# Kernel tuning notes

Hardware: AMD Instinct MI355X
Metric: run time of the kernel (lower is better)

The kernel has to match this reference:

```python
import jax, jax.numpy as jnp
import numpy as np

# ---- static configuration (matches init_kwargs) ----
B = 256              # graph pairs -> 2B graphs total (query/corpus interleaved)
N_PER_GRAPH = 24     # nodes per graph
N_MAX = 32           # max node set size (transport plan side)
E_PER_GRAPH = 200    # edges per graph
E_MAX = 256          # max_edge_set_size
D_EDGE = 256         # edge_feature_dim
D_SINK = 256         # sinkhorn_feature_dim
TEMPERATURE = 0.1
NUM_SINKHORN_ITERS = 20
NOISE_FACTOR = 0.0   # deterministic sinkhorn
CONSISTENCY_WEIGHT = 1.0


def setup_inputs() -> dict:
    rng = np.random.RandomState(0)
    num_graphs = 2 * B
    node_offset = np.arange(num_graphs) * N_PER_GRAPH
    graph_idx = np.repeat(np.arange(num_graphs), N_PER_GRAPH)
    # edges are grouped by graph (standard batched-graph layout)
    from_local = rng.randint(0, N_PER_GRAPH, size=(num_graphs, E_PER_GRAPH))
    to_local = rng.randint(0, N_PER_GRAPH, size=(num_graphs, E_PER_GRAPH))
    from_idx = (from_local + node_offset[:, None]).reshape(-1)
    to_idx = (to_local + node_offset[:, None]).reshape(-1)
    total_edges = num_graphs * E_PER_GRAPH

    key = jax.random.key(0)
    k = jax.random.split(key, 4)
    return {
        "edge_features_enc": jax.random.normal(k[0], (total_edges, D_EDGE), jnp.float32),
        "node_transport_plan": jax.random.uniform(k[1], (B, N_MAX, N_MAX), jnp.float32),
        "W1": jax.random.normal(k[2], (D_EDGE, D_SINK), jnp.float32) / np.sqrt(D_EDGE).astype(np.float32),
        "b1": jnp.zeros((D_SINK,), jnp.float32),
        "W2": jax.random.normal(k[3], (D_SINK, D_SINK), jnp.float32) / np.sqrt(D_SINK).astype(np.float32),
        "b2": jnp.zeros((D_SINK,), jnp.float32),
        "from_idx": jnp.asarray(from_idx, jnp.int32),
        "to_idx": jnp.asarray(to_idx, jnp.int32),
        "graph_idx": jnp.asarray(graph_idx, jnp.int32),
        "query_sizes": jnp.full((B,), N_PER_GRAPH, jnp.int32),
        "corpus_sizes": jnp.full((B,), N_PER_GRAPH, jnp.int32),
    }


def reference(edge_features_enc, node_transport_plan, W1, b1, W2, b2,
              from_idx, to_idx, graph_idx, query_sizes, corpus_sizes):
    num_graphs = 2 * B
    total_edges = from_idx.shape[0]

    # --- get_paired_edge_counts / split_and_stack ---
    g_edge = graph_idx[from_idx]                                   # graph id per edge
    edge_counts = jax.ops.segment_sum(jnp.ones_like(g_edge), g_edge, num_segments=num_graphs)
    edge_offset = jnp.cumsum(edge_counts) - edge_counts            # exclusive prefix
    rank = jnp.arange(total_edges, dtype=jnp.int32) - edge_offset[g_edge]

    stacked = jnp.zeros((num_graphs, E_MAX, D_EDGE), edge_features_enc.dtype)
    stacked = stacked.at[g_edge, rank].set(edge_features_enc)      # [2B, E_MAX, D]
    q_feat, c_feat = stacked[0::2], stacked[1::2]

    # --- sinkhorn_feature_layers (Linear-ReLU-Linear) + size mask ---
    def mlp(x):
        return jax.nn.relu(x @ W1 + b1) @ W2 + b2
    q_feat, c_feat = mlp(q_feat), mlp(c_feat)
    pos = jnp.arange(E_MAX)
    q_feat = q_feat * (pos[None, :] < query_sizes[:, None]).astype(q_feat.dtype)[..., None]
    c_feat = c_feat * (pos[None, :] < corpus_sizes[:, None]).astype(c_feat.dtype)[..., None]

    # --- kronecker_product_on_nodes: local endpoint ids, pad slots -> zero row N_MAX ---
    node_counts = jax.ops.segment_sum(jnp.ones_like(graph_idx), graph_idx, num_segments=num_graphs)
    node_offset = jnp.cumsum(node_counts) - node_counts
    pad = jnp.full((num_graphs, E_MAX), N_MAX, jnp.int32)
    f_loc = pad.at[g_edge, rank].set(from_idx - node_offset[g_edge])
    t_loc = pad.at[g_edge, rank].set(to_idx - node_offset[g_edge])
    fq, fc = f_loc[0::2], f_loc[1::2]
    tq, tc = t_loc[0::2], t_loc[1::2]

    T = jnp.pad(node_transport_plan, ((0, 0), (0, 1), (0, 1)))     # zero row/col for pads
    b = jnp.arange(B)[:, None, None]
    straight = T[b, fq[:, :, None], fc[:, None, :]] * T[b, tq[:, :, None], tc[:, None, :]]
    cross = T[b, fq[:, :, None], tc[:, None, :]] * T[b, tq[:, :, None], fc[:, None, :]]

    # --- sinkhorn_iters (log domain, noise_factor=0) ---
    log_alpha = (straight + cross) / TEMPERATURE                   # [B, E_MAX, E_MAX]
    def step(la, _):
        la = la - jax.nn.logsumexp(la, axis=2, keepdims=True)
        la = la - jax.nn.logsumexp(la, axis=1, keepdims=True)
        return la, None
    log_alpha, _ = jax.lax.scan(step, log_alpha, None, length=NUM_SINKHORN_ITERS)
    plan = jnp.exp(log_alpha)

    # --- feature_alignment_score: -sum(relu(q - P c)) per pair ---
    score = -jax.nn.relu(q_feat - plan @ c_feat).sum(axis=(1, 2))
    return CONSISTENCY_WEIGHT * score
```

## Files before the change

### kernel.cpp

```cpp
#include <hip/hip_runtime.h>

typedef unsigned short ushort_t;
typedef unsigned int uint_t;

typedef float f32x4_t __attribute__((ext_vector_type(4)));
typedef short s16x8_t __attribute__((ext_vector_type(8)));

#define NB   256
#define NG   512
#define NPG  24
#define NMAXI 32
#define EPG  200
#define DD   256
#define L2E_OVER_T 14.426950408889634f

#define PADIDX(i) ((((i) >> 6) * 68) + ((i) & 63))

__device__ __forceinline__ ushort_t f2bf(float f) {
    uint_t u = __float_as_uint(f);
    u += 0x7FFFu + ((u >> 16) & 1u);
    return (ushort_t)(u >> 16);
}
__device__ __forceinline__ float bfhi(uint_t u) { return __uint_as_float(u & 0xFFFF0000u); }
__device__ __forceinline__ float bflo(uint_t u) { return __uint_as_float(u << 16); }

__device__ __forceinline__ float frcp(float x) {
#if __has_builtin(__builtin_amdgcn_rcpf)
    return __builtin_amdgcn_rcpf(x);
#else
    return 1.0f / x;
#endif
}

__global__ __launch_bounds__(256) void prep_w(const float* __restrict__ W1,
                                              const float* __restrict__ W2,
                                              ushort_t* __restrict__ W1T,
                                              ushort_t* __restrict__ W2T)
{
    __shared__ float tile[2][4 * 256];
    const int t = threadIdx.x;
    const int k0 = blockIdx.x * 4;
    #pragma unroll
    for (int i = t; i < 4 * 256; i += 256) {
        tile[0][i] = W1[k0 * 256 + i];
        tile[1][i] = W2[k0 * 256 + i];
    }
    __syncthreads();
    const int n = t;
    #pragma unroll
    for (int m = 0; m < 2; ++m) {
        uint_t p0 = (uint_t)f2bf(tile[m][0 * 256 + n]) | ((uint_t)f2bf(tile[m][1 * 256 + n]) << 16);
        uint_t p1 = (uint_t)f2bf(tile[m][2 * 256 + n]) | ((uint_t)f2bf(tile[m][3 * 256 + n]) << 16);
        ushort_t* dst = (m ? W2T : W1T) + n * 256 + k0;
        uint2 pk; pk.x = p0; pk.y = p1;
        *(uint2*)dst = pk;
    }
}

__global__ __launch_bounds__(256) void mlp_kernel(
    const float* __restrict__ X, const ushort_t* __restrict__ W1T,
    const ushort_t* __restrict__ W2T, const float* __restrict__ b1,
    const float* __restrict__ b2, float* __restrict__ Y)
{
    __shared__ ushort_t sA[64 * 272];
    const int t = threadIdx.x;
    const int blk = blockIdx.x;
    const int lane = t & 63;
    const int w = t >> 6;
    const int quad = lane >> 4;
    const int mrow = lane & 15;

    {
        int r = t >> 2;
        int ch = (t & 3) * 64;
        int rho = blk * 64 + r;
        int g = rho / NPG;
        int e = rho - g * NPG;
        const float* src = X + ((size_t)(g * EPG + e)) * DD + ch;
        ushort_t* dst = &sA[r * 272 + ch];
        #pragma unroll
        for (int i = 0; i < 8; ++i) {
            float4 v0 = *(const float4*)(src + i * 8);
            float4 v1 = *(const float4*)(src + i * 8 + 4);
            uint4 pk;
            pk.x = (uint_t)f2bf(v0.x) | ((uint_t)f2bf(v0.y) << 16);
            pk.y = (uint_t)f2bf(v0.z) | ((uint_t)f2bf(v0.w) << 16);
            pk.z = (uint_t)f2bf(v1.x) | ((uint_t)f2bf(v1.y) << 16);
            pk.w = (uint_t)f2bf(v1.z) | ((uint_t)f2bf(v1.w) << 16);
            *(uint4*)(dst + i * 8) = pk;
        }
    }
    __syncthreads();

    f32x4_t acc[16];
    #pragma unroll
    for (int i = 0; i < 16; ++i) acc[i] = (f32x4_t){0.f, 0.f, 0.f, 0.f};

    #pragma unroll
    for (int k0 = 0; k0 < 256; k0 += 32) {
        s16x8_t a[4], bb[4];
        #pragma unroll
        for (int mt = 0; mt < 4; ++mt)
            a[mt] = *(const s16x8_t*)&sA[(mt * 16 + mrow) * 272 + k0 + quad * 8];
        #pragma unroll
        for (int nt = 0; nt < 4; ++nt)
            bb[nt] = *(const s16x8_t*)(W1T + (size_t)(64 * w + nt * 16 + mrow) * 256 + k0 + quad * 8);
        #pragma unroll
        for (int mt = 0; mt < 4; ++mt) {
            #pragma unroll
            for (int nt = 0; nt < 4; ++nt)
                acc[mt * 4 + nt] = __builtin_amdgcn_mfma_f32_16x16x32_bf16(
                    a[mt], bb[nt], acc[mt * 4 + nt], 0, 0, 0);
        }
    }
    __syncthreads();

    #pragma unroll
    for (int nt = 0; nt < 4; ++nt) {
        int col = 64 * w + nt * 16 + mrow;
        float bias = b1[col];
        #pragma unroll
        for (int mt = 0; mt < 4; ++mt) {
            f32x4_t v = acc[mt * 4 + nt];
            #pragma unroll
            for (int reg = 0; reg < 4; ++reg) {
                int row = mt * 16 + quad * 4 + reg;
                sA[row * 272 + col] = f2bf(fmaxf(v[reg] + bias, 0.f));
            }
        }
    }
    __syncthreads();

    #pragma unroll
    for (int i = 0; i < 16; ++i) acc[i] = (f32x4_t){0.f, 0.f, 0.f, 0.f};

    #pragma unroll
    for (int k0 = 0; k0 < 256; k0 += 32) {
        s16x8_t a[4], bb[4];
        #pragma unroll
        for (int mt = 0; mt < 4; ++mt)
            a[mt] = *(const s16x8_t*)&sA[(mt * 16 + mrow) * 272 + k0 + quad * 8];
        #pragma unroll
        for (int nt = 0; nt < 4; ++nt)
            bb[nt] = *(const s16x8_t*)(W2T + (size_t)(64 * w + nt * 16 + mrow) * 256 + k0 + quad * 8);
        #pragma unroll
        for (int mt = 0; mt < 4; ++mt) {
            #pragma unroll
            for (int nt = 0; nt < 4; ++nt)
                acc[mt * 4 + nt] = __builtin_amdgcn_mfma_f32_16x16x32_bf16(
                    a[mt], bb[nt], acc[mt * 4 + nt], 0, 0, 0);
        }
    }

    #pragma unroll
    for (int nt = 0; nt < 4; ++nt) {
        int col = 64 * w + nt * 16 + mrow;
        float bias = b2[col];
        #pragma unroll
        for (int mt = 0; mt < 4; ++mt) {
            f32x4_t v = acc[mt * 4 + nt];
            #pragma unroll
            for (int reg = 0; reg < 4; ++reg) {
                int row = blk * 64 + mt * 16 + quad * 4 + reg;
                Y[(size_t)row * 256 + col] = v[reg] + bias;
            }
        }
    }
}

__global__ __launch_bounds__(1024, 4) void sink_kernel(
    const float* __restrict__ Tplan, const int* __restrict__ from_idx,
    const int* __restrict__ to_idx, const int* __restrict__ qsz,
    const int* __restrict__ csz, const float* __restrict__ qcf,
    float* __restrict__ out)
{
    const int b = blockIdx.x;
    const int t = threadIdx.x;
    const int r = t >> 2;
    const int q = t & 3;

    __shared__ __align__(16) char ovl[56320];
    __shared__ float ru_s[272], rv_s[272];
    __shared__ float wsum[16];

    float* Tl = (float*)ovl;
    int* fq = (int*)(ovl + 4368);
    int* tq = (int*)(ovl + 5392);
    int* fc = (int*)(ovl + 6416);
    int* tc = (int*)(ovl + 7440);
    float* plan_s = (float*)ovl;
    float* cf_s   = (float*)(ovl + 25600);

    for (int i = t; i < 33 * 33; i += 1024) Tl[i] = 0.f;
    if (t < 256) {
        rv_s[PADIDX(t)] = 1.0f;
        int gq = 2 * b, gc = 2 * b + 1;
        int a = NMAXI, bb = NMAXI, c = NMAXI, d = NMAXI;
        if (t < EPG) {
            a  = from_idx[gq * EPG + t] - gq * NPG;
            bb = to_idx  [gq * EPG + t] - gq * NPG;
            c  = from_idx[gc * EPG + t] - gc * NPG;
            d  = to_idx  [gc * EPG + t] - gc * NPG;
        }
        fq[t] = a; tq[t] = bb; fc[t] = c; tc[t] = d;
    }
    __syncthreads();
    {
        int i = t >> 5, j = t & 31;
        Tl[i * 33 + j] = Tplan[((size_t)b << 10) + t];
    }
    __syncthreads();

    float K[64];
    {
        const float* T1 = &Tl[fq[r] * 33];
        const float* T2 = &Tl[tq[r] * 33];
        #pragma unroll
        for (int o = 0; o < 64; ++o) {
            int cidx = q * 64 + o;
            int f_ = fc[cidx], t_ = tc[cidx];
            float la = T1[f_] * T2[t_] + T1[t_] * T2[f_];
            K[o] = exp2f(la * L2E_OVER_T);
        }
    }
    uint_t KTp[32];
    {
        int j = r;
        int f_ = fc[j], t_ = tc[j];
        #pragma unroll
        for (int oo = 0; oo < 8; ++oo) {
            #pragma unroll
            for (int p2 = 0; p2 < 4; ++p2) {
                int i0 = q * 64 + oo * 8 + p2 * 2;
                const float* A1 = &Tl[fq[i0] * 33];
                const float* A2 = &Tl[tq[i0] * 33];
                float la0 = A1[f_] * A2[t_] + A1[t_] * A2[f_];
                const float* B1 = &Tl[fq[i0 + 1] * 33];
                const float* B2 = &Tl[tq[i0 + 1] * 33];
                float la1 = B1[f_] * B2[t_] + B1[t_] * B2[f_];
                KTp[oo * 4 + p2] = (uint_t)f2bf(exp2f(la0 * L2E_OVER_T))
                                 | ((uint_t)f2bf(exp2f(la1 * L2E_OVER_T)) << 16);
            }
        }
    }

    const float4* rv4 = (const float4*)&rv_s[q * 68];
    const float4* ru4 = (const float4*)&ru_s[q * 68];

    for (int it = 0; it < 20; ++it) {
        float a0 = 0.f, a1 = 0.f, a2 = 0.f, a3 = 0.f;
        #pragma unroll
        for (int c4 = 0; c4 < 16; ++c4) {
            float4 v = rv4[c4];
            a0 += K[c4 * 4 + 0] * v.x;
            a1 += K[c4 * 4 + 1] * v.y;
            a2 += K[c4 * 4 + 2] * v.z;
            a3 += K[c4 * 4 + 3] * v.w;
        }
        float s = (a0 + a1) + (a2 + a3);
        s += __shfl_xor(s, 1);
        s += __shfl_xor(s, 2);
        if (q == 0) ru_s[PADIDX(r)] = frcp(s);
        __syncthreads();
        a0 = a1 = a2 = a3 = 0.f;
        #pragma unroll
        for (int c8 = 0; c8 < 8; ++c8) {
            uint_t k0 = KTp[c8 * 4 + 0], k1 = KTp[c8 * 4 + 1];
            uint_t k2 = KTp[c8 * 4 + 2], k3 = KTp[c8 * 4 + 3];
            float4 u0 = ru4[c8 * 2 + 0];
            float4 u1 = ru4[c8 * 2 + 1];
            a0 += bflo(k0) * u0.x; a1 += bfhi(k0) * u0.y;
            a2 += bflo(k1) * u0.z; a3 += bfhi(k1) * u0.w;
            a0 += bflo(k2) * u1.x; a1 += bfhi(k2) * u1.y;
            a2 += bflo(k3) * u1.z; a3 += bfhi(k3) * u1.w;
        }
        s = (a0 + a1) + (a2 + a3);
        s += __shfl_xor(s, 1);
        s += __shfl_xor(s, 2);
        if (q == 0) rv_s[PADIDX(r)] = frcp(s);
        __syncthreads();
    }

    int nq = qsz[b]; if (nq > 24) nq = 24;
    int nc = csz[b]; if (nc > 24) nc = 24;

    if (q == 0) {
        float rr = ru_s[PADIDX(r)];
        #pragma unroll
        for (int j = 0; j < 24; ++j)
            plan_s[r * 25 + j] = K[j] * rr * rv_s[j];
    }
    if (t < 768) {
        int j = t >> 5, inner = t & 31;
        int c = inner * 8;
        const float* src = qcf + ((size_t)(2 * b + 1) * 24 + j) * 256 + c;
        float4 v0 = *(const float4*)(src);
        float4 v1 = *(const float4*)(src + 4);
        float* dst = cf_s + j * 320 + (c >> 4) * 20 + (c & 15);
        *(float4*)dst = v0;
        *(float4*)(dst + 4) = v1;
    }
    __syncthreads();

    const int rg = t >> 4;
    const int r0 = rg * 4;
    const int m  = t & 15;

    float pc[64];
    #pragma unroll
    for (int i = 0; i < 64; ++i) pc[i] = 0.f;

    for (int j = 0; j < nc; ++j) {
        float p0 = plan_s[(r0 + 0) * 25 + j];
        float p1 = plan_s[(r0 + 1) * 25 + j];
        float p2 = plan_s[(r0 + 2) * 25 + j];
        float p3 = plan_s[(r0 + 3) * 25 + j];
        const float4* cfp = (const float4*)(cf_s + j * 320 + m * 20);
        #pragma unroll
        for (int k = 0; k < 4; ++k) {
            float4 cv = cfp[k];
            pc[ 0 + k * 4 + 0] += p0 * cv.x; pc[ 0 + k * 4 + 1] += p0 * cv.y;
            pc[ 0 + k * 4 + 2] += p0 * cv.z; pc[ 0 + k * 4 + 3] += p0 * cv.w;
            pc[16 + k * 4 + 0] += p1 * cv.x; pc[16 + k * 4 + 1] += p1 * cv.y;
            pc[16 + k * 4 + 2] += p1 * cv.z; pc[16 + k * 4 + 3] += p1 * cv.w;
            pc[32 + k * 4 + 0] += p2 * cv.x; pc[32 + k * 4 + 1] += p2 * cv.y;
            pc[32 + k * 4 + 2] += p2 * cv.z; pc[32 + k * 4 + 3] += p2 * cv.w;
            pc[48 + k * 4 + 0] += p3 * cv.x; pc[48 + k * 4 + 1] += p3 * cv.y;
            pc[48 + k * 4 + 2] += p3 * cv.z; pc[48 + k * 4 + 3] += p3 * cv.w;
        }
    }

    float ssum = 0.f;
    const float* qbase = qcf + (size_t)(2 * b) * 24 * 256;
    #pragma unroll
    for (int i = 0; i < 4; ++i) {
        int row = r0 + i;
        if (row < nq) {
            const float4* qp = (const float4*)(qbase + (size_t)row * 256 + m * 16);
            #pragma unroll
            for (int k = 0; k < 4; ++k) {
                float4 qv = qp[k];
                ssum += fmaxf(qv.x - pc[i * 16 + k * 4 + 0], 0.f);
                ssum += fmaxf(qv.y - pc[i * 16 + k * 4 + 1], 0.f);
                ssum += fmaxf(qv.z - pc[i * 16 + k * 4 + 2], 0.f);
                ssum += fmaxf(qv.w - pc[i * 16 + k * 4 + 3], 0.f);
            }
        } else {
            #pragma unroll
            for (int k = 0; k < 16; ++k) ssum += fmaxf(-pc[i * 16 + k], 0.f);
        }
    }
    ssum += __shfl_xor(ssum, 1);
    ssum += __shfl_xor(ssum, 2);
    ssum += __shfl_xor(ssum, 4);
    ssum += __shfl_xor(ssum, 8);
    ssum += __shfl_xor(ssum, 16);
    ssum += __shfl_xor(ssum, 32);
    if ((t & 63) == 0) wsum[t >> 6] = ssum;
    __syncthreads();
    if (t == 0) {
        float s = 0.f;
        #pragma unroll
        for (int i = 0; i < 16; ++i) s += wsum[i];
        out[b] = -s;
    }
}

extern "C" void kernel_launch(void* const* d_in, const int* in_sizes, int n_in,
                              void* d_out, int out_size, void* d_ws, size_t ws_size,
                              hipStream_t stream)
{
    const float* edge_feat = (const float*)d_in[0];
    const float* tplan     = (const float*)d_in[1];
    const float* W1        = (const float*)d_in[2];
    const float* b1        = (const float*)d_in[3];
    const float* W2        = (const float*)d_in[4];
    const float* b2        = (const float*)d_in[5];
    const int*   from_idx  = (const int*)d_in[6];
    const int*   to_idx    = (const int*)d_in[7];
    const int*   qsz       = (const int*)d_in[9];
    const int*   csz       = (const int*)d_in[10];
    float* out = (float*)d_out;

    char* ws = (char*)d_ws;
    ushort_t* W1T = (ushort_t*)ws;
    ushort_t* W2T = W1T + 65536;
    float* qcf = (float*)(ws + 262144);

    prep_w<<<64, 256, 0, stream>>>(W1, W2, W1T, W2T);
    mlp_kernel<<<192, 256, 0, stream>>>(edge_feat, W1T, W2T, b1, b2, qcf);
    sink_kernel<<<256, 1024, 0, stream>>>(tplan, from_idx, to_idx, qsz, csz, qcf, out);
}
```

Baseline: 286.9 us.

## Tile Sinkhorn kernel matrix 4x16 per thread with single bf16 copy

Each thread now holds a 4-row by 16-column tile of the exp kernel matrix as packed bf16, replacing the separate fp32 row copy and bf16 transposed copy. Row sums reduce across 16 lanes with shuffles. Column sums reduce across lanes, then across waves through a shared scratch buffer and a third barrier. This halves register use and the redundant kernel computation, and drops the occupancy hint in launch bounds, but it adds a barrier and a cross-wave reduction per half-iteration, and row sums now use bf16 values.

```diff
diff --git a/kernel.cpp b/kernel.cpp
--- a/kernel.cpp
+++ b/kernel.cpp
@@ -13,8 +13,6 @@
 #define EPG  200
 #define DD   256
 #define L2E_OVER_T 14.426950408889634f
-
-#define PADIDX(i) ((((i) >> 6) * 68) + ((i) & 63))
 
 __device__ __forceinline__ ushort_t f2bf(float f) {
     uint_t u = __float_as_uint(f);
@@ -168,7 +166,7 @@
     }
 }
 
-__global__ __launch_bounds__(1024, 4) void sink_kernel(
+__global__ __launch_bounds__(1024) void sink_kernel(
     const float* __restrict__ Tplan, const int* __restrict__ from_idx,
     const int* __restrict__ to_idx, const int* __restrict__ qsz,
     const int* __restrict__ csz, const float* __restrict__ qcf,
@@ -176,11 +174,13 @@
 {
     const int b = blockIdx.x;
     const int t = threadIdx.x;
-    const int r = t >> 2;
-    const int q = t & 3;
+    const int R = t >> 4;
+    const int C = t & 15;
+    const int w = t >> 6;
 
     __shared__ __align__(16) char ovl[56320];
-    __shared__ float ru_s[272], rv_s[272];
+    __shared__ float ru_s[260];
+    __shared__ float rv_p[320];
     __shared__ float wsum[16];
 
     float* Tl = (float*)ovl;
@@ -188,12 +188,13 @@
     int* tq = (int*)(ovl + 5392);
     int* fc = (int*)(ovl + 6416);
     int* tc = (int*)(ovl + 7440);
+    float* Vp = (float*)ovl;
     float* plan_s = (float*)ovl;
     float* cf_s   = (float*)(ovl + 25600);
 
     for (int i = t; i < 33 * 33; i += 1024) Tl[i] = 0.f;
+    if (t < 320) rv_p[t] = 1.0f;
     if (t < 256) {
-        rv_s[PADIDX(t)] = 1.0f;
         int gq = 2 * b, gc = 2 * b + 1;
         int a = NMAXI, bb = NMAXI, c = NMAXI, d = NMAXI;
         if (t < EPG) {
@@ -211,84 +212,112 @@
     }
     __syncthreads();
 
-    float K[64];
+    uint_t Kp[4][8];
     {
-        const float* T1 = &Tl[fq[r] * 33];
-        const float* T2 = &Tl[tq[r] * 33];
-        #pragma unroll
-        for (int o = 0; o < 64; ++o) {
-            int cidx = q * 64 + o;
-            int f_ = fc[cidx], t_ = tc[cidx];
-            float la = T1[f_] * T2[t_] + T1[t_] * T2[f_];
-            K[o] = exp2f(la * L2E_OVER_T);
-        }
-    }
-    uint_t KTp[32];
-    {
-        int j = r;
-        int f_ = fc[j], t_ = tc[j];
-        #pragma unroll
-        for (int oo = 0; oo < 8; ++oo) {
-            #pragma unroll
-            for (int p2 = 0; p2 < 4; ++p2) {
-                int i0 = q * 64 + oo * 8 + p2 * 2;
-                const float* A1 = &Tl[fq[i0] * 33];
-                const float* A2 = &Tl[tq[i0] * 33];
-                float la0 = A1[f_] * A2[t_] + A1[t_] * A2[f_];
-                const float* B1 = &Tl[fq[i0 + 1] * 33];
-                const float* B2 = &Tl[tq[i0 + 1] * 33];
-                float la1 = B1[f_] * B2[t_] + B1[t_] * B2[f_];
-                KTp[oo * 4 + p2] = (uint_t)f2bf(exp2f(la0 * L2E_OVER_T))
-                                 | ((uint_t)f2bf(exp2f(la1 * L2E_OVER_T)) << 16);
-            }
-        }
-    }
-
-    const float4* rv4 = (const float4*)&rv_s[q * 68];
-    const float4* ru4 = (const float4*)&ru_s[q * 68];
+        int fcl[16], tcl[16];
+        #pragma unroll
+        for (int o = 0; o < 16; ++o) { fcl[o] = fc[16 * C + o]; tcl[o] = tc[16 * C + o]; }
+        #pragma unroll
+        for (int i = 0; i < 4; ++i) {
+            const float* T1 = &Tl[fq[4 * R + i] * 33];
+            const float* T2 = &Tl[tq[4 * R + i] * 33];
+            #pragma unroll
+            for (int u = 0; u < 8; ++u) {
+                int f0 = fcl[2 * u], t0 = tcl[2 * u];
+                int f1 = fcl[2 * u + 1], t1 = tcl[2 * u + 1];
+                float la0 = T1[f0] * T2[t0] + T1[t0] * T2[f0];
+                float la1 = T1[f1] * T2[t1] + T1[t1] * T2[f1];
+                Kp[i][u] = (uint_t)f2bf(exp2f(la0 * L2E_OVER_T))
+                         | ((uint_t)f2bf(exp2f(la1 * L2E_OVER_T)) << 16);
+            }
+        }
+    }
 
     for (int it = 0; it < 20; ++it) {
-        float a0 = 0.f, a1 = 0.f, a2 = 0.f, a3 = 0.f;
-        #pragma unroll
-        for (int c4 = 0; c4 < 16; ++c4) {
-            float4 v = rv4[c4];
-            a0 += K[c4 * 4 + 0] * v.x;
-            a1 += K[c4 * 4 + 1] * v.y;
-            a2 += K[c4 * 4 + 2] * v.z;
-            a3 += K[c4 * 4 + 3] * v.w;
-        }
-        float s = (a0 + a1) + (a2 + a3);
-        s += __shfl_xor(s, 1);
-        s += __shfl_xor(s, 2);
-        if (q == 0) ru_s[PADIDX(r)] = frcp(s);
+        {
+            float4 rv0 = *(const float4*)&rv_p[20 * C + 0];
+            float4 rv1 = *(const float4*)&rv_p[20 * C + 4];
+            float4 rv2 = *(const float4*)&rv_p[20 * C + 8];
+            float4 rv3 = *(const float4*)&rv_p[20 * C + 12];
+            float pr[4];
+            #pragma unroll
+            for (int i = 0; i < 4; ++i) {
+                float a0 = bflo(Kp[i][0]) * rv0.x + bfhi(Kp[i][0]) * rv0.y;
+                float a1 = bflo(Kp[i][1]) * rv0.z + bfhi(Kp[i][1]) * rv0.w;
+                float a2 = bflo(Kp[i][2]) * rv1.x + bfhi(Kp[i][2]) * rv1.y;
+                float a3 = bflo(Kp[i][3]) * rv1.z + bfhi(Kp[i][3]) * rv1.w;
+                a0 += bflo(Kp[i][4]) * rv2.x + bfhi(Kp[i][4]) * rv2.y;
+                a1 += bflo(Kp[i][5]) * rv2.z + bfhi(Kp[i][5]) * rv2.w;
+                a2 += bflo(Kp[i][6]) * rv3.x + bfhi(Kp[i][6]) * rv3.y;
+                a3 += bflo(Kp[i][7]) * rv3.z + bfhi(Kp[i][7]) * rv3.w;
+                pr[i] = (a0 + a1) + (a2 + a3);
+            }
+            #pragma unroll
+            for (int i = 0; i < 4; ++i) {
+                float s = pr[i];
+                s += __shfl_xor(s, 1);
+                s += __shfl_xor(s, 2);
+                s += __shfl_xor(s, 4);
+                s += __shfl_xor(s, 8);
+                pr[i] = s;
+            }
+            if (C == 0) {
+                #pragma unroll
+                for (int i = 0; i < 4; ++i) ru_s[4 * R + i] = frcp(pr[i]);
+            }
+        }
         __syncthreads();
-        a0 = a1 = a2 = a3 = 0.f;
-        #pragma unroll
-        for (int c8 = 0; c8 < 8; ++c8) {
-            uint_t k0 = KTp[c8 * 4 + 0], k1 = KTp[c8 * 4 + 1];
-            uint_t k2 = KTp[c8 * 4 + 2], k3 = KTp[c8 * 4 + 3];
-            float4 u0 = ru4[c8 * 2 + 0];
-            float4 u1 = ru4[c8 * 2 + 1];
-            a0 += bflo(k0) * u0.x; a1 += bfhi(k0) * u0.y;
-            a2 += bflo(k1) * u0.z; a3 += bfhi(k1) * u0.w;
-            a0 += bflo(k2) * u1.x; a1 += bfhi(k2) * u1.y;
-            a2 += bflo(k3) * u1.z; a3 += bfhi(k3) * u1.w;
-        }
-        s = (a0 + a1) + (a2 + a3);
-        s += __shfl_xor(s, 1);
-        s += __shfl_xor(s, 2);
-        if (q == 0) rv_s[PADIDX(r)] = frcp(s);
+        {
+            float u0 = ru_s[4 * R + 0], u1 = ru_s[4 * R + 1];
+            float u2 = ru_s[4 * R + 2], u3 = ru_s[4 * R + 3];
+            float pc[16];
+            #pragma unroll
+            for (int u = 0; u < 8; ++u) {
+                float e0 = bflo(Kp[0][u]) * u0 + bflo(Kp[1][u]) * u1
+                         + bflo(Kp[2][u]) * u2 + bflo(Kp[3][u]) * u3;
+                float e1 = bfhi(Kp[0][u]) * u0 + bfhi(Kp[1][u]) * u1
+                         + bfhi(Kp[2][u]) * u2 + bfhi(Kp[3][u]) * u3;
+                pc[2 * u] = e0; pc[2 * u + 1] = e1;
+            }
+            #pragma unroll
+            for (int k = 0; k < 16; ++k) {
+                float s = pc[k];
+                s += __shfl_xor(s, 16);
+                s += __shfl_xor(s, 32);
+                pc[k] = s;
+            }
+            if ((t & 63) < 16) {
+                float* dst = &Vp[w * 272 + C * 16];
+                *(float4*)(dst + 0)  = (float4){pc[0], pc[1], pc[2], pc[3]};
+                *(float4*)(dst + 4)  = (float4){pc[4], pc[5], pc[6], pc[7]};
+                *(float4*)(dst + 8)  = (float4){pc[8], pc[9], pc[10], pc[11]};
+                *(float4*)(dst + 12) = (float4){pc[12], pc[13], pc[14], pc[15]};
+            }
+        }
+        __syncthreads();
+        if (t < 256) {
+            float s = 0.f;
+            #pragma unroll
+            for (int ww = 0; ww < 16; ++ww) s += Vp[ww * 272 + t];
+            rv_p[(t >> 4) * 20 + (t & 15)] = frcp(s);
+        }
         __syncthreads();
     }
 
     int nq = qsz[b]; if (nq > 24) nq = 24;
     int nc = csz[b]; if (nc > 24) nc = 24;
 
-    if (q == 0) {
-        float rr = ru_s[PADIDX(r)];
-        #pragma unroll
-        for (int j = 0; j < 24; ++j)
-            plan_s[r * 25 + j] = K[j] * rr * rv_s[j];
+    if (C < 2) {
+        int umax = (C == 0) ? 8 : 4;
+        #pragma unroll
+        for (int i = 0; i < 4; ++i) {
+            float rr = ru_s[4 * R + i];
+            for (int u = 0; u < umax; ++u) {
+                int j = 16 * C + 2 * u;
+                plan_s[(4 * R + i) * 25 + j]     = bflo(Kp[i][u]) * rr * rv_p[20 * C + 2 * u];
+                plan_s[(4 * R + i) * 25 + j + 1] = bfhi(Kp[i][u]) * rr * rv_p[20 * C + 2 * u + 1];
+            }
+        }
     }
     if (t < 768) {
         int j = t >> 5, inner = t & 31;
@@ -302,9 +331,8 @@
     }
     __syncthreads();
 
-    const int rg = t >> 4;
-    const int r0 = rg * 4;
-    const int m  = t & 15;
+    const int r0 = R * 4;
+    const int m  = C;
 
     float pc[64];
     #pragma unroll
```

Measured after the change: 268.2 us. -6.5%, faster.
